# Optimization experiments

Hardware: AMD Instinct MI355X
Metric: run time of the kernel (lower is better)

The kernel has to match this reference:

```python
import jax, jax.numpy as jnp
import numpy as np

INPUT_SHAPE = 640
NUM_CLASSES = 80
STRIDES = (8, 16, 32)
DIS = 2.5 * STRIDES[0]        # center-region half-size (pixels)
EPS = 1e-7
BIG = 1e5                      # penalty for non-(center&inbox) candidates
INF = 1e9                      # effectively excludes a pair from top-k / argmin
BS, MAX_GT, NGT_VALID = 32, 50, 20


def _bce(p, t):
    p = jnp.clip(p, EPS, 1.0 - EPS)
    return -t * jnp.log(p) - (1.0 - t) * jnp.log(1.0 - p)


def _decode(pred, stride):
    # pred [B, 5+nc, l, l] -> decoded [B, l*l, 5+nc] with boxes in pixels (cx,cy,w,h)
    B, C, l, _ = pred.shape
    p = jnp.transpose(pred, (0, 2, 3, 1))          # [B, l, l, C] (row=y, col=x)
    xy = jax.nn.sigmoid(p[..., :2])
    wh = p[..., 2:4]
    objcls = jax.nn.sigmoid(p[..., 4:])
    gx = jnp.arange(l, dtype=p.dtype)[None, :]      # ix varies along width
    gy = jnp.arange(l, dtype=p.dtype)[:, None]      # iy varies along height
    x = (gx + xy[..., 0]) * stride
    y = (gy + xy[..., 1]) * stride
    w = jnp.exp(wh[..., 0]) * stride
    h = jnp.exp(wh[..., 1]) * stride
    out = jnp.concatenate([jnp.stack([x, y, w, h], -1), objcls], -1)
    return out.reshape(B, l * l, C)


def _pairwise_iou(gt, pr):
    # gt [G,4], pr [A,4] in cxcywh -> [G,A]
    g_tl = gt[:, None, :2] - gt[:, None, 2:4] * 0.5
    g_br = gt[:, None, :2] + gt[:, None, 2:4] * 0.5
    p_tl = pr[None, :, :2] - pr[None, :, 2:4] * 0.5
    p_br = pr[None, :, :2] + pr[None, :, 2:4] * 0.5
    wh = jnp.maximum(jnp.minimum(g_br, p_br) - jnp.maximum(g_tl, p_tl), 0.0)
    inter = wh[..., 0] * wh[..., 1]
    union = gt[:, None, 2] * gt[:, None, 3] + pr[None, :, 2] * pr[None, :, 3] - inter
    return inter / jnp.clip(union, 1e-6)


def _region_mask(px, py, cx, cy, hw, hh):
    # anchor center inside (clipped) box around (cx,cy) with half-extents (hw,hh)
    left = jnp.maximum(cx - hw, 0.0)[:, None]
    right = jnp.minimum(cx + hw, float(INPUT_SHAPE))[:, None]
    top = jnp.maximum(cy - hh, 0.0)[:, None]
    bot = jnp.minimum(cy + hh, float(INPUT_SHAPE))[:, None]
    return (px[None] >= left) & (px[None] <= right) & (py[None] >= top) & (py[None] <= bot)


def _per_image(pred, tgt):
    # pred [A, 5+nc] decoded, tgt [G, 5+nc]
    G, A = tgt.shape[0], pred.shape[0]
    valid = tgt[:, 4] == 1.0
    px, py = pred[:, 0], pred[:, 1]
    cx, cy, gw, gh = tgt[:, 0], tgt[:, 1], tgt[:, 2], tgt[:, 3]

    center_m = _region_mask(px, py, cx, cy, DIS, DIS)
    inbox_m = _region_mask(px, py, cx, cy, gw * 0.5, gh * 0.5)
    or_m = (center_m | inbox_m) & valid[:, None]     # candidate anchors
    and_m = center_m & inbox_m & valid[:, None]      # preferred anchors

    iou = _pairwise_iou(tgt[:, :4], pred[:, :4])     # [G, A]
    iou_cost = -jnp.log(iou + 1e-8)

    # pairwise class BCE cost summed over classes, via matmul (one-hot targets)
    pcls = jnp.clip(pred[:, 5:], EPS, 1.0 - EPS)     # [A, nc]
    logp = jnp.log(pcls)
    log1mp = jnp.log(1.0 - pcls)
    tcls = tgt[:, 5:]                                 # [G, nc]
    cls_cost = tcls @ (log1mp - logp).T - log1mp.sum(-1)[None, :]  # [G, A]

    cost = cls_cost + 3.0 * iou_cost + BIG * (~and_m)
    cost_full = jnp.where(valid[:, None], cost, INF)
    cost_sel = jnp.where(or_m, cost, INF)

    # dynamic-k: sum of top-10 candidate IoUs, floored at 1, capped by #and-candidates
    k10 = jax.lax.top_k(iou * or_m.astype(iou.dtype), 10)[0].sum(-1)
    and_cnt = and_m.sum(-1)
    dk = jnp.minimum(jnp.maximum(k10.astype(jnp.int32), 1), jnp.maximum(and_cnt, 1))

    # take 10 lowest-cost anchors per GT, keep the first dk of them
    _, topi = jax.lax.top_k(-cost_sel, 10)            # [G, 10]
    keep = (jnp.arange(10)[None, :] < dk[:, None]) & valid[:, None]
    keep = keep & jnp.take_along_axis(or_m, topi, axis=1)
    assign = jnp.zeros((G, A), jnp.int32).at[jnp.arange(G)[:, None], topi].max(
        keep.astype(jnp.int32)) > 0                    # [G, A] bool

    overlap = assign.sum(0) > 1
    best = jnp.argmin(cost_full, axis=0)              # [A]
    onehot = jnp.arange(G)[:, None] == best[None, :]
    assign = jnp.where(overlap[None, :], onehot, assign)

    fg = assign.any(0)
    l_conf = _bce(pred[:, 4], fg.astype(pred.dtype)).sum()
    l_cls = jnp.sum(jnp.where(assign, cls_cost, 0.0))
    l_reg = jnp.sum(jnp.where(assign, 1.0 - iou ** 2, 0.0))
    return l_reg, l_conf, l_cls, valid.sum()


def setup_inputs() -> dict:
    key = jax.random.key(0)
    k1, k2, k3, k4, k5, k6, k7 = jax.random.split(key, 7)
    p8 = 0.5 * jax.random.normal(k1, (BS, 5 + NUM_CLASSES, 80, 80), jnp.float32)
    p16 = 0.5 * jax.random.normal(k2, (BS, 5 + NUM_CLASSES, 40, 40), jnp.float32)
    p32 = 0.5 * jax.random.normal(k3, (BS, 5 + NUM_CLASSES, 20, 20), jnp.float32)
    # targets: (cx, cy, w, h, valid_flag, one_hot_class)
    cxy = jax.random.uniform(k4, (BS, NGT_VALID, 2), jnp.float32, 32.0, INPUT_SHAPE - 32.0)
    wh = jax.random.uniform(k5, (BS, NGT_VALID, 2), jnp.float32, 16.0, 128.0)
    cls_idx = jax.random.randint(k6, (BS, NGT_VALID), 0, NUM_CLASSES)
    onehot = jax.nn.one_hot(cls_idx, NUM_CLASSES, dtype=jnp.float32)
    flag = jnp.ones((BS, NGT_VALID, 1), jnp.float32)
    valid_rows = jnp.concatenate([cxy, wh, flag, onehot], -1)   # [BS, 20, 85]
    pad = jnp.zeros((BS, MAX_GT - NGT_VALID, 5 + NUM_CLASSES), jnp.float32)
    targets = jnp.concatenate([valid_rows, pad], axis=1)        # [BS, 50, 85]
    return {"p8": p8, "p16": p16, "p32": p32, "targets": targets}


def reference(p8, p16, p32, targets):
    preds = jnp.concatenate(
        [_decode(p8, STRIDES[0]), _decode(p16, STRIDES[1]), _decode(p32, STRIDES[2])],
        axis=1)                                                  # [BS, 8400, 85]
    l_reg, l_conf, l_cls, ng = jax.vmap(_per_image)(preds, targets)
    num_gts = jnp.maximum(ng.sum(), 1).astype(preds.dtype)
    reg_weight = 5.0
    return (reg_weight * l_reg.sum() + l_cls.sum() + l_conf.sum()) / num_gts
```

## Files before the change

kernel.cpp:

```cpp
#include <hip/hip_runtime.h>
#include <math.h>

#define BSZ  32
#define GSZ  50
#define ATOT 8400
#define NCLS 80
#define CDIM 85
#define TPB  256
#define GRIDX ((ATOT + TPB - 1) / TPB)
#define NPART (GRIDX * BSZ)
#define MAXC 512

#define EPSF 1e-7f
#define BIGF 100000.0f
#define INFF 1000000000.0f
#define IMGF 640.0f
#define DISF 20.0f
#define LOGEPS_HI -15.942385f

__device__ __forceinline__ float sigm(float z){ return 1.0f/(1.0f+expf(-z)); }
__device__ __forceinline__ float clampp(float s){ return fminf(fmaxf(s, EPSF), 1.f-EPSF); }
__device__ __forceinline__ float log1msig(float z){
  return fmaxf(-logf(1.f + expf(z)), LOGEPS_HI);
}

__device__ __forceinline__ const float* chan_ptr(const float* __restrict__ p8,
                                                 const float* __restrict__ p16,
                                                 const float* __restrict__ p32,
                                                 int b, int a, int ch){
  if (a < 6400) return p8  + ((size_t)(b*CDIM + ch))*6400 + a;
  if (a < 8000) return p16 + ((size_t)(b*CDIM + ch))*1600 + (a-6400);
  return p32 + ((size_t)(b*CDIM + ch))*400 + (a-8000);
}

__device__ __forceinline__ void compute_pair(
  float cx, float cy, float gw, float gh,
  float px, float py, float pw, float ph,
  float z, float slog,
  float& cost, float& iou, bool& orm, bool& andm, float& clsc)
{
  float hw = gw*0.5f, hh = gh*0.5f;
  bool cm = (px >= fmaxf(cx-DISF,0.f)) && (px <= fminf(cx+DISF,IMGF)) &&
            (py >= fmaxf(cy-DISF,0.f)) && (py <= fminf(cy+DISF,IMGF));
  bool im = (px >= fmaxf(cx-hw,0.f)) && (px <= fminf(cx+hw,IMGF)) &&
            (py >= fmaxf(cy-hh,0.f)) && (py <= fminf(cy+hh,IMGF));
  orm = cm || im;  andm = cm && im;
  float phw = pw*0.5f, phh = ph*0.5f;
  float wx = fmaxf(fminf(cx+hw, px+phw) - fmaxf(cx-hw, px-phw), 0.f);
  float wy = fmaxf(fminf(cy+hh, py+phh) - fmaxf(cy-hh, py-phh), 0.f);
  float inter = wx*wy;
  float uni   = gw*gh + pw*ph - inter;
  iou = inter / fmaxf(uni, 1e-6f);
  clsc = -z - slog;
  cost = clsc + 3.f*(-logf(iou + 1e-8f)) + (andm ? 0.f : BIGF);
}

__global__ void k_prep(const float* __restrict__ tgt, int* __restrict__ cidx){
  int t = blockIdx.x*blockDim.x + threadIdx.x;
  if (t >= BSZ*GSZ) return;
  const float* T = tgt + (size_t)t*CDIM;
  int best = 0; float bv = T[5];
  for (int c = 1; c < NCLS; c++){
    float v = T[5+c];
    if (v > bv){ bv = v; best = c; }
  }
  cidx[t] = best;
}

__global__ void k_decode(const float* __restrict__ p8, const float* __restrict__ p16,
                         const float* __restrict__ p32,
                         float* __restrict__ bx, float* __restrict__ by,
                         float* __restrict__ bw, float* __restrict__ bh,
                         float* __restrict__ obj, float* __restrict__ slog,
                         unsigned long long* __restrict__ bits){
  int t = blockIdx.x*blockDim.x + threadIdx.x;
  int sub = t & 3;
  int g   = t >> 2;
  int b = g / (ATOT/4);
  int q = g % (ATOT/4);
  int a0 = q*4;
  const float* base; int l; float fs; int aL;
  if (a0 < 6400){ base = p8;  l = 80; fs = 8.f;  aL = a0; }
  else if (a0 < 8000){ base = p16; l = 40; fs = 16.f; aL = a0-6400; }
  else { base = p32; l = 20; fs = 32.f; aL = a0-8000; }
  int l2 = l*l;
  int cs = l2 >> 2;
  const float4* p4 = (const float4*)(base + (size_t)b*CDIM*l2) + (aL >> 2);

  float4 S = make_float4(0.f,0.f,0.f,0.f);
  for (int c = 5+sub; c < CDIM; c += 4){
    float4 v = p4[c*cs];
    S.x += log1msig(v.x); S.y += log1msig(v.y);
    S.z += log1msig(v.z); S.w += log1msig(v.w);
  }
  #pragma unroll
  for (int m = 1; m <= 2; m <<= 1){
    S.x += __shfl_xor(S.x, m, 64);
    S.y += __shfl_xor(S.y, m, 64);
    S.z += __shfl_xor(S.z, m, 64);
    S.w += __shfl_xor(S.w, m, 64);
  }

  int i = aL / l, j = aL % l;
  float fi = (float)i;
  uint4 z4 = make_uint4(0u,0u,0u,0u);
  if (sub == 0){
    float4 v0 = p4[0];
    float4 v4 = p4[4*cs];
    ((float4*)bx)[g]  = make_float4(((float)(j  )+sigm(v0.x))*fs, ((float)(j+1)+sigm(v0.y))*fs,
                                    ((float)(j+2)+sigm(v0.z))*fs, ((float)(j+3)+sigm(v0.w))*fs);
    ((float4*)obj)[g] = make_float4(sigm(v4.x), sigm(v4.y), sigm(v4.z), sigm(v4.w));
    ((uint4*)bits)[2*g] = z4;
  } else if (sub == 1){
    float4 v1 = p4[cs];
    ((float4*)by)[g]   = make_float4((fi+sigm(v1.x))*fs, (fi+sigm(v1.y))*fs,
                                     (fi+sigm(v1.z))*fs, (fi+sigm(v1.w))*fs);
    ((float4*)slog)[g] = S;
  } else if (sub == 2){
    float4 v2 = p4[2*cs];
    ((float4*)bw)[g] = make_float4(expf(v2.x)*fs, expf(v2.y)*fs, expf(v2.z)*fs, expf(v2.w)*fs);
    ((uint4*)bits)[2*g+1] = z4;
  } else {
    float4 v3 = p4[3*cs];
    ((float4*)bh)[g] = make_float4(expf(v3.x)*fs, expf(v3.y)*fs, expf(v3.z)*fs, expf(v3.w)*fs);
  }
}

__global__ void k_assign(const float* __restrict__ p8, const float* __restrict__ p16,
                         const float* __restrict__ p32, const float* __restrict__ tgt,
                         const int* __restrict__ cidx,
                         const float* __restrict__ bx, const float* __restrict__ by,
                         const float* __restrict__ bw, const float* __restrict__ bh,
                         const float* __restrict__ slog,
                         unsigned long long* __restrict__ bits){
  int g = blockIdx.x, b = blockIdx.y;
  const float* T = tgt + ((size_t)b*GSZ + g)*CDIM;
  if (T[4] != 1.0f) return;
  float cx = T[0], cy = T[1], gw = T[2], gh = T[3];
  float hw = gw*0.5f, hh = gh*0.5f;
  float cL = fmaxf(cx-DISF,0.f), cR = fminf(cx+DISF,IMGF);
  float cT = fmaxf(cy-DISF,0.f), cB = fminf(cy+DISF,IMGF);
  float iL = fmaxf(cx-hw,0.f),  iR = fminf(cx+hw,IMGF);
  float iT = fmaxf(cy-hh,0.f),  iB = fminf(cy+hh,IMGF);
  float gArea = gw*gh;
  int ch = 5 + cidx[b*GSZ + g];
  int t = threadIdx.x;
  int lane = t & 63, wave = t >> 6;

  const float* BX = bx + (size_t)b*ATOT;
  const float* BY = by + (size_t)b*ATOT;
  const float* BW = bw + (size_t)b*ATOT;
  const float* BH = bh + (size_t)b*ATOT;
  const float* SL = slog + (size_t)b*ATOT;

  __shared__ int cand[MAXC];
  __shared__ int ncand_sh, nand_sh;
  if (t == 0){ ncand_sh = 0; nand_sh = 0; }
  __syncthreads();
  for (int a = t; a < ATOT; a += TPB){
    float px = BX[a], py = BY[a];
    bool cm = (px >= cL) && (px <= cR) && (py >= cT) && (py <= cB);
    bool im = (px >= iL) && (px <= iR) && (py >= iT) && (py <= iB);
    if (cm || im){
      int pos = atomicAdd(&ncand_sh, 1);
      if (pos < MAXC) cand[pos] = a | ((cm && im) ? 0x10000 : 0);
      if (cm && im) atomicAdd(&nand_sh, 1);
    }
  }
  __syncthreads();
  int nc = ncand_sh < MAXC ? ncand_sh : MAXC;
  int and_cnt = nand_sh;

  float lc[10]; int li[10]; float lio[10];
  #pragma unroll
  for (int k = 0; k < 10; k++){ lc[k] = 3.0e38f; li[k] = -1; lio[k] = -1.f; }

  for (int c = t; c < nc; c += TPB){
    int packed = cand[c];
    int a = packed & 0xFFFF;
    bool andm = (packed & 0x10000) != 0;
    float px = BX[a], py = BY[a];
    float pw = BW[a], ph = BH[a];
    float phw = pw*0.5f, phh = ph*0.5f;
    float wx = fmaxf(fminf(cx+hw, px+phw) - fmaxf(cx-hw, px-phw), 0.f);
    float wy = fmaxf(fminf(cy+hh, py+phh) - fmaxf(cy-hh, py-phh), 0.f);
    float inter = wx*wy;
    float iou = inter / fmaxf(gArea + pw*ph - inter, 1e-6f);
    float z = *chan_ptr(p8, p16, p32, b, a, ch);
    float clsc = -z - SL[a];
    float cost = clsc + 3.f*(-logf(iou + 1e-8f)) + (andm ? 0.f : BIGF);
    {
      float v = cost; int vi = a;
      #pragma unroll
      for (int k = 0; k < 10; k++){
        if (v < lc[k] || (v == lc[k] && (unsigned)vi < (unsigned)li[k])){
          float tv = lc[k]; int ti = li[k];
          lc[k] = v; li[k] = vi; v = tv; vi = ti;
        }
      }
    }
    if (iou > lio[9]){
      float v = iou;
      #pragma unroll
      for (int k = 0; k < 10; k++){
        if (v > lio[k]){ float tv = lio[k]; lio[k] = v; v = tv; }
      }
    }
  }

  float mc[10]; int mi[10]; float mio[10];
  {
    int hp = 0;
    #pragma unroll
    for (int r = 0; r < 10; r++){
      float v  = (hp < 10) ? lc[hp] : 3.4e38f;
      int  idx = (hp < 10) ? li[hp] : -1;
      int  wl  = lane;
      #pragma unroll
      for (int s2 = 32; s2 > 0; s2 >>= 1){
        float v2 = __shfl_xor(v, s2, 64);
        int   i2 = __shfl_xor(idx, s2, 64);
        int   l2 = __shfl_xor(wl, s2, 64);
        if (v2 < v || (v2 == v && (unsigned)i2 < (unsigned)idx)){
          v = v2; idx = i2; wl = l2;
        }
      }
      mc[r] = v; mi[r] = idx;
      if (lane == wl) hp++;
    }
    int hq = 0;
    #pragma unroll
    for (int r = 0; r < 10; r++){
      float v = (hq < 10) ? lio[hq] : -2.f;
      int  wl = lane;
      #pragma unroll
      for (int s2 = 32; s2 > 0; s2 >>= 1){
        float v2 = __shfl_xor(v, s2, 64);
        int   l2 = __shfl_xor(wl, s2, 64);
        if (v2 > v || (v2 == v && l2 < wl)){ v = v2; wl = l2; }
      }
      mio[r] = v;
      if (lane == wl) hq++;
    }
  }

  __shared__ float smc[4*10]; __shared__ int smi[4*10]; __shared__ float smio[4*10];
  if (lane == 0){
    #pragma unroll
    for (int k = 0; k < 10; k++){
      smc[wave*10+k] = mc[k]; smi[wave*10+k] = mi[k]; smio[wave*10+k] = mio[k];
    }
  }
  __syncthreads();

  if (t == 0){
    float k10 = 0.f;
    {
      int h[4] = {0,0,0,0};
      for (int r = 0; r < 10; r++){
        float v = -2.f; int w = -1;
        for (int q = 0; q < 4; q++){
          if (h[q] < 10){
            float vq = smio[q*10+h[q]];
            if (vq > v){ v = vq; w = q; }
          }
        }
        if (w >= 0) h[w]++;
        k10 += fmaxf(v, 0.f);
      }
    }
    int dk = (int)k10;
    if (dk < 1) dk = 1;
    int ub = and_cnt > 1 ? and_cnt : 1;
    if (dk > ub) dk = ub;
    int h[4] = {0,0,0,0};
    for (int r = 0; r < dk && r < 10; r++){
      float v = 3.4e38f; int idx = -1; int w = -1;
      for (int q = 0; q < 4; q++){
        if (h[q] < 10){
          float vq = smc[q*10+h[q]]; int iq = smi[q*10+h[q]];
          if (vq < v || (vq == v && (unsigned)iq < (unsigned)idx)){
            v = vq; idx = iq; w = q;
          }
        }
      }
      if (idx < 0) break;
      h[w]++;
      atomicOr(&bits[(size_t)b*ATOT + idx], 1ull << g);
    }
  }
}

__global__ void k_loss(const float* __restrict__ p8, const float* __restrict__ p16,
                       const float* __restrict__ p32, const float* __restrict__ tgt,
                       const int* __restrict__ cidx,
                       const float* __restrict__ bx, const float* __restrict__ by,
                       const float* __restrict__ bw, const float* __restrict__ bh,
                       const float* __restrict__ obj, const float* __restrict__ slog,
                       const unsigned long long* __restrict__ bits,
                       float* __restrict__ partials){
  int b = blockIdx.y;
  int a = blockIdx.x*TPB + threadIdx.x;
  __shared__ float gcx[GSZ], gcy[GSZ], ggw[GSZ], ggh[GSZ], gval[GSZ];
  __shared__ int gci[GSZ];
  for (int k = threadIdx.x; k < GSZ; k += TPB){
    const float* T = tgt + ((size_t)b*GSZ + k)*CDIM;
    gcx[k] = T[0]; gcy[k] = T[1]; ggw[k] = T[2]; ggh[k] = T[3]; gval[k] = T[4];
    gci[k] = cidx[b*GSZ + k];
  }
  __syncthreads();

  float contrib = 0.f;
  if (a < ATOT){
    size_t t = (size_t)b*ATOT + a;
    unsigned long long m = bits[t];
    float px = bx[t], py = by[t], pw = bw[t], ph = bh[t], sl = slog[t];
    if (__builtin_popcountll(m) > 1){
      float bestc = INFF; int bestg = 0;
      for (int g = 0; g < GSZ; g++){
        float c = INFF;
        if (gval[g] == 1.0f){
          float z = *chan_ptr(p8, p16, p32, b, a, 5+gci[g]);
          float iou, clsc; bool orm, andm;
          compute_pair(gcx[g], gcy[g], ggw[g], ggh[g], px, py, pw, ph, z, sl,
                       c, iou, orm, andm, clsc);
        }
        if (c < bestc){ bestc = c; bestg = g; }
      }
      m = 1ull << bestg;
    }
    bool fg = (m != 0ull);
    float o = clampp(obj[t]);
    contrib = fg ? -logf(o) : -logf(1.f - o);
    while (m){
      int g = __builtin_ctzll(m);
      m &= m - 1;
      float z = *chan_ptr(p8, p16, p32, b, a, 5+gci[g]);
      float c, iou, clsc; bool orm, andm;
      compute_pair(gcx[g], gcy[g], ggw[g], ggh[g], px, py, pw, ph, z, sl,
                   c, iou, orm, andm, clsc);
      contrib += clsc + 5.f*(1.f - iou*iou);
    }
  }

  #pragma unroll
  for (int s2 = 32; s2 > 0; s2 >>= 1) contrib += __shfl_xor(contrib, s2, 64);
  __shared__ float wsum[4];
  if ((threadIdx.x & 63) == 0) wsum[threadIdx.x >> 6] = contrib;
  __syncthreads();
  if (threadIdx.x == 0)
    partials[blockIdx.y*GRIDX + blockIdx.x] = wsum[0]+wsum[1]+wsum[2]+wsum[3];
}

__global__ void k_final(const float* __restrict__ partials,
                        const float* __restrict__ tgt, float* __restrict__ out){
  int t = threadIdx.x;
  float s = 0.f;
  for (int i = t; i < NPART; i += TPB) s += partials[i];
  int n = 0;
  for (int i = t; i < BSZ*GSZ; i += TPB)
    n += (tgt[(size_t)i*CDIM + 4] == 1.0f) ? 1 : 0;
  __shared__ float sh[TPB]; __shared__ int shn[TPB];
  sh[t] = s; shn[t] = n;
  __syncthreads();
  for (int st = TPB/2; st > 0; st >>= 1){
    if (t < st){ sh[t] += sh[t+st]; shn[t] += shn[t+st]; }
    __syncthreads();
  }
  if (t == 0){
    int nn = shn[0] < 1 ? 1 : shn[0];
    out[0] = sh[0] / (float)nn;
  }
}

extern "C" void kernel_launch(void* const* d_in, const int* in_sizes, int n_in,
                              void* d_out, int out_size, void* d_ws, size_t ws_size,
                              hipStream_t stream) {
  const float* p8  = (const float*)d_in[0];
  const float* p16 = (const float*)d_in[1];
  const float* p32 = (const float*)d_in[2];
  const float* tgt = (const float*)d_in[3];
  float* out = (float*)d_out;

  const size_t BA = (size_t)BSZ*ATOT;
  float* bx   = (float*)d_ws;
  float* by   = bx + BA;
  float* bw   = by + BA;
  float* bh   = bw + BA;
  float* obj  = bh + BA;
  float* slog = obj + BA;
  unsigned long long* bits = (unsigned long long*)(slog + BA);
  int* cidx = (int*)(bits + BA);
  float* partials = (float*)(cidx + BSZ*GSZ);

  dim3 blk(TPB);
  k_prep  <<<dim3((BSZ*GSZ + TPB-1)/TPB), blk, 0, stream>>>(tgt, cidx);
  k_decode<<<dim3((unsigned)(BA/TPB)), blk, 0, stream>>>(p8, p16, p32,
                                                   bx, by, bw, bh, obj, slog, bits);
  k_assign<<<dim3(GSZ, BSZ), blk, 0, stream>>>(p8, p16, p32, tgt, cidx,
                                               bx, by, bw, bh, slog, bits);
  k_loss  <<<dim3(GRIDX, BSZ), blk, 0, stream>>>(p8, p16, p32, tgt, cidx,
                                               bx, by, bw, bh, obj, slog, bits, partials);
  k_final <<<1, blk, 0, stream>>>(partials, tgt, out);
}
```

Before: 189.6 us.

## Fold class-index prep into decode kernel and use 8 lanes per anchor group

Removes the separate k_prep launch by having one extra block of k_decode compute the per-target class indices. The decode kernel now assigns 8 threads per group of 4 anchors instead of 4, so each thread sums 10 class channels in a fully unrolled loop, and the output writes are spread one per lane. This trims launch overhead and raises memory-level parallelism, at the cost of twice as many threads and an extra shuffle stage. A single block now scans all 1600 targets serially.

```diff
diff --git a/kernel.cpp b/kernel.cpp
--- a/kernel.cpp
+++ b/kernel.cpp
@@ -10,6 +10,7 @@
 #define GRIDX ((ATOT + TPB - 1) / TPB)
 #define NPART (GRIDX * BSZ)
 #define MAXC 512
+#define DECBLK ((BSZ*ATOT*8/4) / TPB)
 
 #define EPSF 1e-7f
 #define BIGF 100000.0f
@@ -55,27 +56,28 @@
   cost = clsc + 3.f*(-logf(iou + 1e-8f)) + (andm ? 0.f : BIGF);
 }
 
-__global__ void k_prep(const float* __restrict__ tgt, int* __restrict__ cidx){
-  int t = blockIdx.x*blockDim.x + threadIdx.x;
-  if (t >= BSZ*GSZ) return;
-  const float* T = tgt + (size_t)t*CDIM;
-  int best = 0; float bv = T[5];
-  for (int c = 1; c < NCLS; c++){
-    float v = T[5+c];
-    if (v > bv){ bv = v; best = c; }
-  }
-  cidx[t] = best;
-}
-
 __global__ void k_decode(const float* __restrict__ p8, const float* __restrict__ p16,
-                         const float* __restrict__ p32,
+                         const float* __restrict__ p32, const float* __restrict__ tgt,
                          float* __restrict__ bx, float* __restrict__ by,
                          float* __restrict__ bw, float* __restrict__ bh,
                          float* __restrict__ obj, float* __restrict__ slog,
-                         unsigned long long* __restrict__ bits){
+                         unsigned long long* __restrict__ bits,
+                         int* __restrict__ cidx){
+  if (blockIdx.x == DECBLK){
+    for (int t = threadIdx.x; t < BSZ*GSZ; t += TPB){
+      const float* T = tgt + (size_t)t*CDIM;
+      int best = 0; float bv = T[5];
+      for (int c = 1; c < NCLS; c++){
+        float v = T[5+c];
+        if (v > bv){ bv = v; best = c; }
+      }
+      cidx[t] = best;
+    }
+    return;
+  }
   int t = blockIdx.x*blockDim.x + threadIdx.x;
-  int sub = t & 3;
-  int g   = t >> 2;
+  int sub = t & 7;
+  int g   = t >> 3;
   int b = g / (ATOT/4);
   int q = g % (ATOT/4);
   int a0 = q*4;
@@ -88,13 +90,14 @@
   const float4* p4 = (const float4*)(base + (size_t)b*CDIM*l2) + (aL >> 2);
 
   float4 S = make_float4(0.f,0.f,0.f,0.f);
-  for (int c = 5+sub; c < CDIM; c += 4){
-    float4 v = p4[c*cs];
+  #pragma unroll
+  for (int k = 0; k < 10; k++){
+    float4 v = p4[(5 + sub + 8*k)*cs];
     S.x += log1msig(v.x); S.y += log1msig(v.y);
     S.z += log1msig(v.z); S.w += log1msig(v.w);
   }
   #pragma unroll
-  for (int m = 1; m <= 2; m <<= 1){
+  for (int m = 1; m <= 4; m <<= 1){
     S.x += __shfl_xor(S.x, m, 64);
     S.y += __shfl_xor(S.y, m, 64);
     S.z += __shfl_xor(S.z, m, 64);
@@ -104,25 +107,32 @@
   int i = aL / l, j = aL % l;
   float fi = (float)i;
   uint4 z4 = make_uint4(0u,0u,0u,0u);
-  if (sub == 0){
-    float4 v0 = p4[0];
-    float4 v4 = p4[4*cs];
-    ((float4*)bx)[g]  = make_float4(((float)(j  )+sigm(v0.x))*fs, ((float)(j+1)+sigm(v0.y))*fs,
-                                    ((float)(j+2)+sigm(v0.z))*fs, ((float)(j+3)+sigm(v0.w))*fs);
-    ((float4*)obj)[g] = make_float4(sigm(v4.x), sigm(v4.y), sigm(v4.z), sigm(v4.w));
-    ((uint4*)bits)[2*g] = z4;
-  } else if (sub == 1){
-    float4 v1 = p4[cs];
-    ((float4*)by)[g]   = make_float4((fi+sigm(v1.x))*fs, (fi+sigm(v1.y))*fs,
-                                     (fi+sigm(v1.z))*fs, (fi+sigm(v1.w))*fs);
-    ((float4*)slog)[g] = S;
-  } else if (sub == 2){
-    float4 v2 = p4[2*cs];
-    ((float4*)bw)[g] = make_float4(expf(v2.x)*fs, expf(v2.y)*fs, expf(v2.z)*fs, expf(v2.w)*fs);
-    ((uint4*)bits)[2*g+1] = z4;
-  } else {
-    float4 v3 = p4[3*cs];
-    ((float4*)bh)[g] = make_float4(expf(v3.x)*fs, expf(v3.y)*fs, expf(v3.z)*fs, expf(v3.w)*fs);
+  switch (sub){
+    case 0: {
+      float4 v = p4[0];
+      ((float4*)bx)[g] = make_float4(((float)(j  )+sigm(v.x))*fs, ((float)(j+1)+sigm(v.y))*fs,
+                                     ((float)(j+2)+sigm(v.z))*fs, ((float)(j+3)+sigm(v.w))*fs);
+      break; }
+    case 1: {
+      float4 v = p4[cs];
+      ((float4*)by)[g] = make_float4((fi+sigm(v.x))*fs, (fi+sigm(v.y))*fs,
+                                     (fi+sigm(v.z))*fs, (fi+sigm(v.w))*fs);
+      break; }
+    case 2: {
+      float4 v = p4[2*cs];
+      ((float4*)bw)[g] = make_float4(expf(v.x)*fs, expf(v.y)*fs, expf(v.z)*fs, expf(v.w)*fs);
+      break; }
+    case 3: {
+      float4 v = p4[3*cs];
+      ((float4*)bh)[g] = make_float4(expf(v.x)*fs, expf(v.y)*fs, expf(v.z)*fs, expf(v.w)*fs);
+      break; }
+    case 4: {
+      float4 v = p4[4*cs];
+      ((float4*)obj)[g] = make_float4(sigm(v.x), sigm(v.y), sigm(v.z), sigm(v.w));
+      break; }
+    case 5: ((float4*)slog)[g] = S; break;
+    case 6: ((uint4*)bits)[2*g] = z4; break;
+    default: ((uint4*)bits)[2*g+1] = z4; break;
   }
 }
 
@@ -394,9 +404,8 @@
   float* partials = (float*)(cidx + BSZ*GSZ);
 
   dim3 blk(TPB);
-  k_prep  <<<dim3((BSZ*GSZ + TPB-1)/TPB), blk, 0, stream>>>(tgt, cidx);
-  k_decode<<<dim3((unsigned)(BA/TPB)), blk, 0, stream>>>(p8, p16, p32,
-                                                   bx, by, bw, bh, obj, slog, bits);
+  k_decode<<<dim3(DECBLK + 1), blk, 0, stream>>>(p8, p16, p32, tgt,
+                                                 bx, by, bw, bh, obj, slog, bits, cidx);
   k_assign<<<dim3(GSZ, BSZ), blk, 0, stream>>>(p8, p16, p32, tgt, cidx,
                                                bx, by, bw, bh, slog, bits);
   k_loss  <<<dim3(GRIDX, BSZ), blk, 0, stream>>>(p8, p16, p32, tgt, cidx,
```

New measurement: 228.4 us. 20.5% more time.
